# Kernel optimization log

Measured on AMD Instinct MI355X. Metric: run time of the kernel, lower is better.

The kernel has to match this reference:

```python
import jax, jax.numpy as jnp
import numpy as np

N = 50000      # nodes
DEG = 16       # avg degree
E = N * DEG    # edges
F_IN = 256
F_OUT = 128
ALPHA = 0.2    # leaky-relu slope


def setup_inputs() -> dict:
    key = jax.random.key(0)
    k1, k2, k3, k4, k5, k6 = jax.random.split(key, 6)
    x = jax.random.normal(k1, (N, F_IN), dtype=jnp.float32)
    # edges sorted by source (required by the module's `m` construction)
    src = jnp.repeat(jnp.arange(N, dtype=jnp.int32), DEG)
    dst = jax.random.randint(k2, (E,), 0, N, dtype=jnp.int32)
    edge = jnp.stack([src, dst])  # (2, E)
    s_w = 1.414 * np.sqrt(2.0 / (F_IN + F_OUT))   # xavier_normal gain=1.414
    s_a = 1.414 * np.sqrt(2.0 / (1 + 2 * F_OUT))
    W_high = jax.random.normal(k3, (F_IN, F_OUT), jnp.float32) * s_w
    W_low = jax.random.normal(k4, (F_IN, F_OUT), jnp.float32) * s_w
    a_high = jax.random.normal(k5, (1, 2 * F_OUT), jnp.float32) * s_a
    a_low = jax.random.normal(k6, (1, 2 * F_OUT), jnp.float32) * s_a
    return {"x": x, "edge": edge, "W_high": W_high, "W_low": W_low,
            "a_high": a_high, "a_low": a_low}


def _leaky(v):
    return jnp.where(v >= 0, v, ALPHA * v)


def _elu6(v):
    return jnp.minimum(jnp.where(v > 0, v, jnp.expm1(v)), 6.0)


def reference(x, edge, W_high, W_low, a_high, a_low):
    src, dst = edge[0], edge[1]
    n = x.shape[0]
    h_hi = x @ W_high            # (N, F_OUT)
    h_lo = x @ W_low

    # per-edge attention logits: a . [h[src], h[dst]]
    a_hi_s, a_hi_d = a_high[0, :F_OUT], a_high[0, F_OUT:]
    a_lo_s, a_lo_d = a_low[0, :F_OUT], a_low[0, F_OUT:]
    logit_hi = (h_hi @ a_hi_s)[src] + (h_hi @ a_hi_d)[dst]   # (E,)
    logit_lo = (h_lo @ a_lo_s)[src] + (h_lo @ a_lo_d)[dst]
    e_hi = jnp.exp(-_leaky(logit_hi))
    e_lo = jnp.exp(-_leaky(logit_lo))

    # sparse rowsum: spmm(edge, e, [N,N], ones) == segment_sum over src
    rowsum_hi = jax.ops.segment_sum(e_hi, src, num_segments=n)[:, None]
    rowsum_lo = jax.ops.segment_sum(e_lo, src, num_segments=n)[:, None]

    # relu6 (dropout p=0 / eval mode -> identity)
    e_hi = jnp.clip(e_hi, 0.0, 6.0)
    e_lo = jnp.clip(e_lo, 0.0, 6.0)

    # per-edge features, then m @ (.) == segment-sum of edge features by source
    he_hi = h_hi[src] + h_hi[dst]                # (E, F_OUT)
    he_lo = h_lo[src] - h_lo[dst]
    hn_hi = jax.ops.segment_sum(he_hi, src, num_segments=n)  # (N, F_OUT)
    hn_lo = jax.ops.segment_sum(he_lo, src, num_segments=n)

    # spmm(edge, e, [N,N], hn): row i sums e_ij * hn[j] over its edges
    hp_hi = jax.ops.segment_sum(e_hi[:, None] * hn_hi[dst], src, num_segments=n)
    hp_lo = jax.ops.segment_sum(e_lo[:, None] * hn_lo[dst], src, num_segments=n)

    hp_hi = hp_hi / (rowsum_hi + 1e-16)
    hp_lo = hp_lo / (rowsum_lo + 1e-16)
    h_prime = 0.5 * (hp_hi + hp_lo)
    return _elu6(h_prime)  # concat=True branch
```

## Files before the change

kernel.cpp:

```cpp
#include <hip/hip_runtime.h>
#include <hip/hip_bf16.h>
#include <math.h>

#define NN    50000
#define DEG   16
#define FIN   256
#define FOUT  128
#define EE    (NN * DEG)
#define ALPHA 0.2f

#define BM 64
#define BN 256

#define SLW 32

typedef __hip_bfloat16 bf16;
typedef _Float16 f16;
typedef __attribute__((ext_vector_type(8))) _Float16 f16x8;
typedef __attribute__((ext_vector_type(8))) short short8;
typedef __attribute__((ext_vector_type(4))) float f32x4;

__global__ __launch_bounds__(256) void split_w_kernel(
    const float* __restrict__ Wh, const float* __restrict__ Wl,
    bf16* __restrict__ Wcat2)
{
    const int k = blockIdx.x;
    const int n = threadIdx.x;
    const float w = (n < FOUT) ? Wh[(size_t)k * FOUT + n]
                               : Wl[(size_t)k * FOUT + (n - FOUT)];
    const bf16 hi = __float2bfloat16(w);
    const bf16 lo = __float2bfloat16(w - __bfloat162float(hi));
    Wcat2[(size_t)n * 512 + k]       = hi;
    Wcat2[(size_t)n * 512 + 256 + k] = lo;
}

__global__ __launch_bounds__(256) void gemm_mfma_kernel(
    const float* __restrict__ x, const bf16* __restrict__ Wcat2,
    const float* __restrict__ a_high, const float* __restrict__ a_low,
    f16* __restrict__ h16, float* __restrict__ sd_s, float* __restrict__ sd_d)
{
    __shared__ bf16 Ah[BM * 32];
    __shared__ bf16 Al[BM * 32];
    __shared__ bf16 Ba[BN * 32];
    __shared__ bf16 Bb[BN * 32];

    const int t    = threadIdx.x;
    const int lane = t & 63;
    const int w    = t >> 6;
    const int r0   = blockIdx.x * BM;

    f32x4 acc[4][4] = {};

    const int arow = t >> 2;
    const float* xsrc = x + (size_t)min(r0 + arow, NN - 1) * FIN + (t & 3) * 8;
    const int awaddr = arow * 64 + ((((t & 3)) + (arow >> 1)) & 3) * 16;

    int bro[4], bsl[4];
#pragma unroll
    for (int i = 0; i < 4; ++i) {
        const int idx = t + i * 256;
        bro[i] = idx >> 2;
        bsl[i] = ((idx & 3) - (bro[i] >> 1)) & 3;
    }

    const int lr = lane & 15, lg = lane >> 4;

    float4 xa = *(const float4*)(xsrc + 0);
    float4 xb = *(const float4*)(xsrc + 4);

#pragma unroll
    for (int s = 0; s < 8; ++s) {
        const int c0 = s * 32;
        __syncthreads();

#pragma unroll
        for (int i = 0; i < 4; ++i) {
            __builtin_amdgcn_global_load_lds(
                (const __attribute__((address_space(1))) void*)
                    (Wcat2 + (size_t)bro[i] * 512 + c0 + bsl[i] * 8),
                (__attribute__((address_space(3))) void*)((char*)Ba + (t + i * 256) * 16),
                16, 0, 0);
            __builtin_amdgcn_global_load_lds(
                (const __attribute__((address_space(1))) void*)
                    (Wcat2 + (size_t)bro[i] * 512 + 256 + c0 + bsl[i] * 8),
                (__attribute__((address_space(3))) void*)((char*)Bb + (t + i * 256) * 16),
                16, 0, 0);
        }

        {
            short8 hi8, lo8;
            const float f[8] = {xa.x, xa.y, xa.z, xa.w, xb.x, xb.y, xb.z, xb.w};
#pragma unroll
            for (int j = 0; j < 8; ++j) {
                const bf16 h = __float2bfloat16(f[j]);
                const bf16 l = __float2bfloat16(f[j] - __bfloat162float(h));
                ((bf16*)&hi8)[j] = h;
                ((bf16*)&lo8)[j] = l;
            }
            *(short8*)((char*)Ah + awaddr) = hi8;
            *(short8*)((char*)Al + awaddr) = lo8;
        }

        if (s < 7) {
            xa = *(const float4*)(xsrc + (s + 1) * 32 + 0);
            xb = *(const float4*)(xsrc + (s + 1) * 32 + 4);
        }

        __syncthreads();

        short8 fh[4], wa[4], wb[4], fl[4];
#pragma unroll
        for (int mi = 0; mi < 4; ++mi) {
            const int row  = mi * 16 + lr;
            const int slot = (lg + (row >> 1)) & 3;
            fh[mi] = *(const short8*)((const char*)Ah + row * 64 + slot * 16);
        }
#pragma unroll
        for (int ni = 0; ni < 4; ++ni) {
            const int row  = w * 64 + ni * 16 + lr;
            const int slot = (lg + (row >> 1)) & 3;
            wa[ni] = *(const short8*)((const char*)Ba + row * 64 + slot * 16);
        }
#pragma unroll
        for (int mi = 0; mi < 4; ++mi)
#pragma unroll
            for (int ni = 0; ni < 4; ++ni)
                acc[mi][ni] = __builtin_amdgcn_mfma_f32_16x16x32_bf16(
                    fh[mi], wa[ni], acc[mi][ni], 0, 0, 0);
#pragma unroll
        for (int ni = 0; ni < 4; ++ni) {
            const int row  = w * 64 + ni * 16 + lr;
            const int slot = (lg + (row >> 1)) & 3;
            wb[ni] = *(const short8*)((const char*)Bb + row * 64 + slot * 16);
        }
#pragma unroll
        for (int mi = 0; mi < 4; ++mi)
#pragma unroll
            for (int ni = 0; ni < 4; ++ni)
                acc[mi][ni] = __builtin_amdgcn_mfma_f32_16x16x32_bf16(
                    fh[mi], wb[ni], acc[mi][ni], 0, 0, 0);
#pragma unroll
        for (int mi = 0; mi < 4; ++mi) {
            const int row  = mi * 16 + lr;
            const int slot = (lg + (row >> 1)) & 3;
            fl[mi] = *(const short8*)((const char*)Al + row * 64 + slot * 16);
        }
#pragma unroll
        for (int mi = 0; mi < 4; ++mi)
#pragma unroll
            for (int ni = 0; ni < 4; ++ni)
                acc[mi][ni] = __builtin_amdgcn_mfma_f32_16x16x32_bf16(
                    fl[mi], wa[ni], acc[mi][ni], 0, 0, 0);
    }

    const int slc_base = (w < 2) ? w * 4 : (w - 2) * 4;
    const int off      = ((w < 2) ? 0 : 16) + lr;
#pragma unroll
    for (int mi = 0; mi < 4; ++mi) {
        const int rowb = r0 + mi * 16 + lg * 4;
#pragma unroll
        for (int r = 0; r < 4; ++r) {
            const int row = rowb + r;
            if (row >= NN) continue;
#pragma unroll
            for (int ni = 0; ni < 4; ++ni)
                h16[((size_t)(slc_base + ni) * NN + row) * SLW + off] =
                    (f16)acc[mi][ni][r];
        }
    }

    __syncthreads();

    const float* aa = (w < 2) ? a_high : a_low;
    const int cb = (w < 2) ? w * 64 : (w - 2) * 64;
    float as_[4], ad_[4];
#pragma unroll
    for (int ni = 0; ni < 4; ++ni) {
        as_[ni] = aa[cb + ni * 16 + lr];
        ad_[ni] = aa[FOUT + cb + ni * 16 + lr];
    }
    float* sred = (float*)Ah;
#pragma unroll
    for (int mi = 0; mi < 4; ++mi)
#pragma unroll
        for (int r = 0; r < 4; ++r) {
            float ps = 0.f, pd = 0.f;
#pragma unroll
            for (int ni = 0; ni < 4; ++ni) {
                ps += acc[mi][ni][r] * as_[ni];
                pd += acc[mi][ni][r] * ad_[ni];
            }
#pragma unroll
            for (int o = 1; o < 16; o <<= 1) {
                ps += __shfl_xor(ps, o);
                pd += __shfl_xor(pd, o);
            }
            if (lr == 0) {
                const int row = mi * 16 + lg * 4 + r;
                sred[(w * 2 + 0) * 64 + row] = ps;
                sred[(w * 2 + 1) * 64 + row] = pd;
            }
        }
    __syncthreads();
    if (t < 64) {
        const int row = r0 + t;
        if (row < NN) {
            const float s_hi = sred[0 * 64 + t] + sred[2 * 64 + t];
            const float d_hi = sred[1 * 64 + t] + sred[3 * 64 + t];
            const float s_lo = sred[4 * 64 + t] + sred[6 * 64 + t];
            const float d_lo = sred[5 * 64 + t] + sred[7 * 64 + t];
            ((float2*)sd_s)[row] = make_float2(s_hi, s_lo);
            ((float2*)sd_d)[row] = make_float2(d_hi, d_lo);
        }
    }
}

__global__ __launch_bounds__(256) void weight_kernel(
    const int* __restrict__ dst, const float* __restrict__ sd_s,
    const float* __restrict__ sd_d, uint2* __restrict__ ewd)
{
    const int wid  = (blockIdx.x * 256 + threadIdx.x) >> 6;
    const int lane = threadIdx.x & 63;
    if (wid >= NN) return;

    const int e    = lane & 15;
    const int d_my = dst[wid * DEG + e];
    const bool whi = (lane & 16) == 0;
    const float2 s2 = ((const float2*)sd_s)[wid];
    const float2 dd = ((const float2*)sd_d)[d_my];
    const float l   = whi ? (s2.x + dd.x) : (s2.y + dd.y);
    const float ev  = __expf(-(l >= 0.f ? l : ALPHA * l));

    float rs = ev;
    rs += __shfl_xor(rs, 1);
    rs += __shfl_xor(rs, 2);
    rs += __shfl_xor(rs, 4);
    rs += __shfl_xor(rs, 8);
    const float wn = fminf(ev, 6.f) / (rs + 1e-16f);
    const float wl = __shfl(wn, e + 16);

    if (lane < 16) {
        const f16 wh16 = (f16)wn, wl16 = (f16)wl;
        const unsigned a = *(const unsigned short*)&wh16;
        const unsigned b = *(const unsigned short*)&wl16;
        ewd[wid * DEG + e] = make_uint2((unsigned)d_my, a | (b << 16));
    }
}

__global__ __launch_bounds__(320) void hn_slice_kernel(
    const f16* __restrict__ h16, const int* __restrict__ dst,
    f16* __restrict__ hn16)
{
    const int sl    = blockIdx.x & 7;
    const int chunk = blockIdx.x >> 3;
    const int wv    = threadIdx.x >> 6;
    const int lane  = threadIdx.x & 63;
    const int k     = lane >> 2;
    const int c     = lane & 3;
    const int n     = (chunk * 5 + wv) * 16 + k;

    const char* hsl = (const char*)(h16 + (size_t)sl * NN * SLW);
    const float sgn = (c < 2) ? 1.f : -1.f;
    const unsigned coff = (unsigned)c * 16u;
    const unsigned noff = (unsigned)n * 64u + coff;

    const int* db = dst + n * DEG;
    const f16x8 own = *(const f16x8*)(hsl + noff);

    float acc[8] = {};
#pragma unroll
    for (int t = 0; t < DEG; ++t) {
        const unsigned d = (unsigned)db[t];
        const f16x8 g = *(const f16x8*)(hsl + (d * 64u + coff));
#pragma unroll
        for (int j = 0; j < 8; ++j) acc[j] = fmaf(sgn, (float)g[j], acc[j]);
    }
    f16x8 o;
#pragma unroll
    for (int j = 0; j < 8; ++j) o[j] = (f16)fmaf((float)own[j], 16.f, acc[j]);
    *(f16x8*)((char*)(hn16 + (size_t)sl * NN * SLW) + noff) = o;
}

__global__ __launch_bounds__(320) void out_slice_kernel(
    const f16* __restrict__ hn16, const uint2* __restrict__ ewd,
    float* __restrict__ out)
{
    const int sl    = blockIdx.x & 7;
    const int chunk = blockIdx.x >> 3;
    const int wv    = threadIdx.x >> 6;
    const int lane  = threadIdx.x & 63;
    const int k     = lane >> 2;
    const int c     = lane & 3;
    const int n     = (chunk * 5 + wv) * 16 + k;
    const bool chi  = (c < 2);

    const char* hsl = (const char*)(hn16 + (size_t)sl * NN * SLW);
    const unsigned coff = (unsigned)c * 16u;
    const uint2* eb = ewd + n * DEG;

    float acc[8] = {};
#pragma unroll
    for (int t = 0; t < DEG; ++t) {
        const uint2 rec = eb[t];
        const unsigned short wu = chi ? (unsigned short)(rec.y & 0xffffu)
                                      : (unsigned short)(rec.y >> 16);
        const float w = (float)(*(const f16*)&wu);
        const f16x8 g = *(const f16x8*)(hsl + (rec.x * 64u + coff));
#pragma unroll
        for (int j = 0; j < 8; ++j) acc[j] = fmaf(w, (float)g[j], acc[j]);
    }

    float4 v0, v1;
#pragma unroll
    for (int j = 0; j < 8; ++j) {
        const float p = __shfl_xor(acc[j], 2);
        float v = 0.5f * (acc[j] + p);
        v = (v > 0.f) ? v : (__expf(v) - 1.f);
        v = fminf(v, 6.f);
        if (j < 4) ((float*)&v0)[j] = v; else ((float*)&v1)[j - 4] = v;
    }
    if (chi) {
        float* op = out + (size_t)n * FOUT + sl * 16 + c * 8;
        *(float4*)op       = v0;
        *(float4*)(op + 4) = v1;
    }
}

extern "C" void kernel_launch(void* const* d_in, const int* in_sizes, int n_in,
                              void* d_out, int out_size, void* d_ws, size_t ws_size,
                              hipStream_t stream)
{
    const float* x      = (const float*)d_in[0];
    const int*   edge   = (const int*)d_in[1];
    const float* Wh     = (const float*)d_in[2];
    const float* Wl     = (const float*)d_in[3];
    const float* a_high = (const float*)d_in[4];
    const float* a_low  = (const float*)d_in[5];
    const int*   dstv   = edge + EE;

    char* ws = (char*)d_ws;
    f16*   h16   = (f16*)ws;
    f16*   hn16  = (f16*)(ws + 25600000);
    bf16*  Wcat2 = (bf16*)(ws + 51200000);
    float* sd_s  = (float*)(ws + 51600000);
    float* sd_d  = (float*)(ws + 52000000);
    uint2* ewd   = (uint2*)(ws + 52400000);

    split_w_kernel<<<dim3(256), dim3(256), 0, stream>>>(Wh, Wl, Wcat2);
    gemm_mfma_kernel<<<dim3((NN + BM - 1) / BM), dim3(256), 0, stream>>>(
        x, Wcat2, a_high, a_low, h16, sd_s, sd_d);
    weight_kernel<<<dim3((NN + 3) / 4), dim3(256), 0, stream>>>(dstv, sd_s, sd_d, ewd);
    hn_slice_kernel<<<dim3(8 * 625), dim3(320), 0, stream>>>(h16, dstv, hn16);
    out_slice_kernel<<<dim3(8 * 625), dim3(320), 0, stream>>>(hn16, ewd, (float*)d_out);
}
```

Measured before the change: 139.3 us.

## Double-buffer GEMM tiles, split edge records, and halve per-lane edge work in gathers

The GEMM now double-buffers its LDS tiles, so the next K-slice's weight (global_load_lds) and activation loads are issued before the current slice's MFMAs, with one barrier per iteration. The packed (dst, weight) edge records become a separate 16-bit destination array and a 32-bit packed-weight array, cutting index bytes and allowing vector loads of 8 indices. In the hn and out gather kernels each node's 16 edges are split across two lanes with a shuffle reduction, doubling the grid to expose more memory-level parallelism. The cost is more shuffles, twice the LDS in the GEMM, and 16-bit node indices that only hold while N stays below 65536.

```diff
diff --git a/kernel.cpp b/kernel.cpp
--- a/kernel.cpp
+++ b/kernel.cpp
@@ -19,6 +19,8 @@
 typedef __attribute__((ext_vector_type(8))) _Float16 f16x8;
 typedef __attribute__((ext_vector_type(8))) short short8;
 typedef __attribute__((ext_vector_type(4))) float f32x4;
+typedef __attribute__((ext_vector_type(8))) unsigned short u16x8;
+typedef __attribute__((ext_vector_type(8))) unsigned int u32x8;
 
 __global__ __launch_bounds__(256) void split_w_kernel(
     const float* __restrict__ Wh, const float* __restrict__ Wl,
@@ -39,10 +41,10 @@
     const float* __restrict__ a_high, const float* __restrict__ a_low,
     f16* __restrict__ h16, float* __restrict__ sd_s, float* __restrict__ sd_d)
 {
-    __shared__ bf16 Ah[BM * 32];
-    __shared__ bf16 Al[BM * 32];
-    __shared__ bf16 Ba[BN * 32];
-    __shared__ bf16 Bb[BN * 32];
+    __shared__ bf16 Ah[2][BM * 32];
+    __shared__ bf16 Al[2][BM * 32];
+    __shared__ bf16 Ba[2][BN * 32];
+    __shared__ bf16 Bb[2][BN * 32];
 
     const int t    = threadIdx.x;
     const int lane = t & 63;
@@ -67,27 +69,41 @@
 
     float4 xa = *(const float4*)(xsrc + 0);
     float4 xb = *(const float4*)(xsrc + 4);
+#pragma unroll
+    for (int i = 0; i < 4; ++i) {
+        __builtin_amdgcn_global_load_lds(
+            (const __attribute__((address_space(1))) void*)
+                (Wcat2 + (size_t)bro[i] * 512 + 0 + bsl[i] * 8),
+            (__attribute__((address_space(3))) void*)((char*)Ba[0] + (t + i * 256) * 16),
+            16, 0, 0);
+        __builtin_amdgcn_global_load_lds(
+            (const __attribute__((address_space(1))) void*)
+                (Wcat2 + (size_t)bro[i] * 512 + 256 + 0 + bsl[i] * 8),
+            (__attribute__((address_space(3))) void*)((char*)Bb[0] + (t + i * 256) * 16),
+            16, 0, 0);
+    }
+    {
+        short8 hi8, lo8;
+        const float f[8] = {xa.x, xa.y, xa.z, xa.w, xb.x, xb.y, xb.z, xb.w};
+#pragma unroll
+        for (int j = 0; j < 8; ++j) {
+            const bf16 h = __float2bfloat16(f[j]);
+            const bf16 l = __float2bfloat16(f[j] - __bfloat162float(h));
+            ((bf16*)&hi8)[j] = h;
+            ((bf16*)&lo8)[j] = l;
+        }
+        *(short8*)((char*)Ah[0] + awaddr) = hi8;
+        *(short8*)((char*)Al[0] + awaddr) = lo8;
+    }
+    xa = *(const float4*)(xsrc + 32 + 0);
+    xb = *(const float4*)(xsrc + 32 + 4);
+    __syncthreads();
 
 #pragma unroll
     for (int s = 0; s < 8; ++s) {
-        const int c0 = s * 32;
-        __syncthreads();
-
-#pragma unroll
-        for (int i = 0; i < 4; ++i) {
-            __builtin_amdgcn_global_load_lds(
-                (const __attribute__((address_space(1))) void*)
-                    (Wcat2 + (size_t)bro[i] * 512 + c0 + bsl[i] * 8),
-                (__attribute__((address_space(3))) void*)((char*)Ba + (t + i * 256) * 16),
-                16, 0, 0);
-            __builtin_amdgcn_global_load_lds(
-                (const __attribute__((address_space(1))) void*)
-                    (Wcat2 + (size_t)bro[i] * 512 + 256 + c0 + bsl[i] * 8),
-                (__attribute__((address_space(3))) void*)((char*)Bb + (t + i * 256) * 16),
-                16, 0, 0);
-        }
-
-        {
+        const int cur = s & 1, nxt = cur ^ 1;
+
+        if (s < 7) {
             short8 hi8, lo8;
             const float f[8] = {xa.x, xa.y, xa.z, xa.w, xb.x, xb.y, xb.z, xb.w};
 #pragma unroll
@@ -97,29 +113,41 @@
                 ((bf16*)&hi8)[j] = h;
                 ((bf16*)&lo8)[j] = l;
             }
-            *(short8*)((char*)Ah + awaddr) = hi8;
-            *(short8*)((char*)Al + awaddr) = lo8;
-        }
-
-        if (s < 7) {
-            xa = *(const float4*)(xsrc + (s + 1) * 32 + 0);
-            xb = *(const float4*)(xsrc + (s + 1) * 32 + 4);
-        }
-
-        __syncthreads();
+            *(short8*)((char*)Ah[nxt] + awaddr) = hi8;
+            *(short8*)((char*)Al[nxt] + awaddr) = lo8;
+
+            const int c1 = (s + 1) * 32;
+#pragma unroll
+            for (int i = 0; i < 4; ++i) {
+                __builtin_amdgcn_global_load_lds(
+                    (const __attribute__((address_space(1))) void*)
+                        (Wcat2 + (size_t)bro[i] * 512 + c1 + bsl[i] * 8),
+                    (__attribute__((address_space(3))) void*)((char*)Ba[nxt] + (t + i * 256) * 16),
+                    16, 0, 0);
+                __builtin_amdgcn_global_load_lds(
+                    (const __attribute__((address_space(1))) void*)
+                        (Wcat2 + (size_t)bro[i] * 512 + 256 + c1 + bsl[i] * 8),
+                    (__attribute__((address_space(3))) void*)((char*)Bb[nxt] + (t + i * 256) * 16),
+                    16, 0, 0);
+            }
+            if (s < 6) {
+                xa = *(const float4*)(xsrc + (s + 2) * 32 + 0);
+                xb = *(const float4*)(xsrc + (s + 2) * 32 + 4);
+            }
+        }
 
         short8 fh[4], wa[4], wb[4], fl[4];
 #pragma unroll
         for (int mi = 0; mi < 4; ++mi) {
             const int row  = mi * 16 + lr;
             const int slot = (lg + (row >> 1)) & 3;
-            fh[mi] = *(const short8*)((const char*)Ah + row * 64 + slot * 16);
+            fh[mi] = *(const short8*)((const char*)Ah[cur] + row * 64 + slot * 16);
         }
 #pragma unroll
         for (int ni = 0; ni < 4; ++ni) {
             const int row  = w * 64 + ni * 16 + lr;
             const int slot = (lg + (row >> 1)) & 3;
-            wa[ni] = *(const short8*)((const char*)Ba + row * 64 + slot * 16);
+            wa[ni] = *(const short8*)((const char*)Ba[cur] + row * 64 + slot * 16);
         }
 #pragma unroll
         for (int mi = 0; mi < 4; ++mi)
@@ -131,7 +159,7 @@
         for (int ni = 0; ni < 4; ++ni) {
             const int row  = w * 64 + ni * 16 + lr;
             const int slot = (lg + (row >> 1)) & 3;
-            wb[ni] = *(const short8*)((const char*)Bb + row * 64 + slot * 16);
+            wb[ni] = *(const short8*)((const char*)Bb[cur] + row * 64 + slot * 16);
         }
 #pragma unroll
         for (int mi = 0; mi < 4; ++mi)
@@ -143,7 +171,7 @@
         for (int mi = 0; mi < 4; ++mi) {
             const int row  = mi * 16 + lr;
             const int slot = (lg + (row >> 1)) & 3;
-            fl[mi] = *(const short8*)((const char*)Al + row * 64 + slot * 16);
+            fl[mi] = *(const short8*)((const char*)Al[cur] + row * 64 + slot * 16);
         }
 #pragma unroll
         for (int mi = 0; mi < 4; ++mi)
@@ -151,6 +179,8 @@
             for (int ni = 0; ni < 4; ++ni)
                 acc[mi][ni] = __builtin_amdgcn_mfma_f32_16x16x32_bf16(
                     fl[mi], wa[ni], acc[mi][ni], 0, 0, 0);
+
+        __syncthreads();
     }
 
     const int slc_base = (w < 2) ? w * 4 : (w - 2) * 4;
@@ -179,7 +209,7 @@
         as_[ni] = aa[cb + ni * 16 + lr];
         ad_[ni] = aa[FOUT + cb + ni * 16 + lr];
     }
-    float* sred = (float*)Ah;
+    float* sred = (float*)Ah[0];
 #pragma unroll
     for (int mi = 0; mi < 4; ++mi)
 #pragma unroll
@@ -217,7 +247,8 @@
 
 __global__ __launch_bounds__(256) void weight_kernel(
     const int* __restrict__ dst, const float* __restrict__ sd_s,
-    const float* __restrict__ sd_d, uint2* __restrict__ ewd)
+    const float* __restrict__ sd_d, unsigned short* __restrict__ d16,
+    unsigned int* __restrict__ w32)
 {
     const int wid  = (blockIdx.x * 256 + threadIdx.x) >> 6;
     const int lane = threadIdx.x & 63;
@@ -243,83 +274,95 @@
         const f16 wh16 = (f16)wn, wl16 = (f16)wl;
         const unsigned a = *(const unsigned short*)&wh16;
         const unsigned b = *(const unsigned short*)&wl16;
-        ewd[wid * DEG + e] = make_uint2((unsigned)d_my, a | (b << 16));
+        d16[wid * DEG + e] = (unsigned short)d_my;
+        w32[wid * DEG + e] = a | (b << 16);
     }
 }
 
 __global__ __launch_bounds__(320) void hn_slice_kernel(
-    const f16* __restrict__ h16, const int* __restrict__ dst,
+    const f16* __restrict__ h16, const unsigned short* __restrict__ d16,
     f16* __restrict__ hn16)
 {
     const int sl    = blockIdx.x & 7;
     const int chunk = blockIdx.x >> 3;
     const int wv    = threadIdx.x >> 6;
     const int lane  = threadIdx.x & 63;
-    const int k     = lane >> 2;
-    const int c     = lane & 3;
-    const int n     = (chunk * 5 + wv) * 16 + k;
+    const int k     = lane >> 3;
+    const int c     = (lane >> 1) & 3;
+    const int hf    = lane & 1;
+    const int n     = (chunk * 5 + wv) * 8 + k;
 
     const char* hsl = (const char*)(h16 + (size_t)sl * NN * SLW);
     const float sgn = (c < 2) ? 1.f : -1.f;
     const unsigned coff = (unsigned)c * 16u;
     const unsigned noff = (unsigned)n * 64u + coff;
 
-    const int* db = dst + n * DEG;
+    const u16x8 d8 = *(const u16x8*)(d16 + n * DEG + hf * 8);
     const f16x8 own = *(const f16x8*)(hsl + noff);
 
     float acc[8] = {};
 #pragma unroll
-    for (int t = 0; t < DEG; ++t) {
-        const unsigned d = (unsigned)db[t];
+    for (int t = 0; t < 8; ++t) {
+        const unsigned d = (unsigned)d8[t];
         const f16x8 g = *(const f16x8*)(hsl + (d * 64u + coff));
 #pragma unroll
         for (int j = 0; j < 8; ++j) acc[j] = fmaf(sgn, (float)g[j], acc[j]);
     }
-    f16x8 o;
-#pragma unroll
-    for (int j = 0; j < 8; ++j) o[j] = (f16)fmaf((float)own[j], 16.f, acc[j]);
-    *(f16x8*)((char*)(hn16 + (size_t)sl * NN * SLW) + noff) = o;
+#pragma unroll
+    for (int j = 0; j < 8; ++j) acc[j] += __shfl_xor(acc[j], 1);
+
+    if (hf == 0) {
+        f16x8 o;
+#pragma unroll
+        for (int j = 0; j < 8; ++j) o[j] = (f16)fmaf((float)own[j], 16.f, acc[j]);
+        *(f16x8*)((char*)(hn16 + (size_t)sl * NN * SLW) + noff) = o;
+    }
 }
 
 __global__ __launch_bounds__(320) void out_slice_kernel(
-    const f16* __restrict__ hn16, const uint2* __restrict__ ewd,
-    float* __restrict__ out)
+    const f16* __restrict__ hn16, const unsigned short* __restrict__ d16,
+    const unsigned int* __restrict__ w32, float* __restrict__ out)
 {
     const int sl    = blockIdx.x & 7;
     const int chunk = blockIdx.x >> 3;
     const int wv    = threadIdx.x >> 6;
     const int lane  = threadIdx.x & 63;
-    const int k     = lane >> 2;
-    const int c     = lane & 3;
-    const int n     = (chunk * 5 + wv) * 16 + k;
+    const int k     = lane >> 3;
+    const int c     = (lane >> 1) & 3;
+    const int hf    = lane & 1;
+    const int n     = (chunk * 5 + wv) * 8 + k;
     const bool chi  = (c < 2);
 
     const char* hsl = (const char*)(hn16 + (size_t)sl * NN * SLW);
     const unsigned coff = (unsigned)c * 16u;
-    const uint2* eb = ewd + n * DEG;
+
+    const u16x8 d8 = *(const u16x8*)(d16 + n * DEG + hf * 8);
+    const u32x8 w8 = *(const u32x8*)(w32 + n * DEG + hf * 8);
 
     float acc[8] = {};
 #pragma unroll
-    for (int t = 0; t < DEG; ++t) {
-        const uint2 rec = eb[t];
-        const unsigned short wu = chi ? (unsigned short)(rec.y & 0xffffu)
-                                      : (unsigned short)(rec.y >> 16);
+    for (int t = 0; t < 8; ++t) {
+        const unsigned wp = w8[t];
+        const unsigned short wu = chi ? (unsigned short)(wp & 0xffffu)
+                                      : (unsigned short)(wp >> 16);
         const float w = (float)(*(const f16*)&wu);
-        const f16x8 g = *(const f16x8*)(hsl + (rec.x * 64u + coff));
+        const f16x8 g = *(const f16x8*)(hsl + ((unsigned)d8[t] * 64u + coff));
 #pragma unroll
         for (int j = 0; j < 8; ++j) acc[j] = fmaf(w, (float)g[j], acc[j]);
     }
+#pragma unroll
+    for (int j = 0; j < 8; ++j) acc[j] += __shfl_xor(acc[j], 1);
 
     float4 v0, v1;
 #pragma unroll
     for (int j = 0; j < 8; ++j) {
-        const float p = __shfl_xor(acc[j], 2);
+        const float p = __shfl_xor(acc[j], 4);
         float v = 0.5f * (acc[j] + p);
         v = (v > 0.f) ? v : (__expf(v) - 1.f);
         v = fminf(v, 6.f);
         if (j < 4) ((float*)&v0)[j] = v; else ((float*)&v1)[j - 4] = v;
     }
-    if (chi) {
+    if (chi && hf == 0) {
         float* op = out + (size_t)n * FOUT + sl * 16 + c * 8;
         *(float4*)op       = v0;
         *(float4*)(op + 4) = v1;
@@ -342,14 +385,15 @@
     f16*   h16   = (f16*)ws;
     f16*   hn16  = (f16*)(ws + 25600000);
     bf16*  Wcat2 = (bf16*)(ws + 51200000);
-    float* sd_s  = (float*)(ws + 51600000);
-    float* sd_d  = (float*)(ws + 52000000);
-    uint2* ewd   = (uint2*)(ws + 52400000);
+    float* sd_s  = (float*)(ws + 51800000);
+    float* sd_d  = (float*)(ws + 52200000);
+    unsigned short* d16 = (unsigned short*)(ws + 52600000);
+    unsigned int*   w32 = (unsigned int*)(ws + 54400000);
 
     split_w_kernel<<<dim3(256), dim3(256), 0, stream>>>(Wh, Wl, Wcat2);
     gemm_mfma_kernel<<<dim3((NN + BM - 1) / BM), dim3(256), 0, stream>>>(
         x, Wcat2, a_high, a_low, h16, sd_s, sd_d);
-    weight_kernel<<<dim3((NN + 3) / 4), dim3(256), 0, stream>>>(dstv, sd_s, sd_d, ewd);
-    hn_slice_kernel<<<dim3(8 * 625), dim3(320), 0, stream>>>(h16, dstv, hn16);
-    out_slice_kernel<<<dim3(8 * 625), dim3(320), 0, stream>>>(hn16, ewd, (float*)d_out);
-}
+    weight_kernel<<<dim3((NN + 3) / 4), dim3(256), 0, stream>>>(dstv, sd_s, sd_d, d16, w32);
+    hn_slice_kernel<<<dim3(8 * 1250), dim3(320), 0, stream>>>(h16, d16, hn16);
+    out_slice_kernel<<<dim3(8 * 1250), dim3(320), 0, stream>>>(hn16, d16, w32, (float*)d_out);
+}
```

Measured after the change: 130.3 us. 1.07x faster.
